# Optimization experiments

Measured on AMD Instinct MI355X. Metric: run time of the kernel, lower is better.

Reference implementation:

```python
import jax, jax.numpy as jnp
import numpy as np
import math

B, S, D, H, DFF, V = 8, 512, 512, 8, 2048, 32000
EPS = 1e-5

def _pe_table(max_len, d):
    pos = jnp.arange(max_len, dtype=jnp.float32)[:, None]
    i = jnp.arange(d)
    exponent = (2 * (i // 2)).astype(jnp.float32) / d
    angle = pos / jnp.power(10000.0, exponent)[None, :]
    return jnp.where(i % 2 == 0, jnp.sin(angle), jnp.cos(angle))

def _ln(x, g, b):
    mu = jnp.mean(x, -1, keepdims=True)
    var = jnp.mean((x - mu) ** 2, -1, keepdims=True)
    return g * (x - mu) * jax.lax.rsqrt(var + EPS) + b

def setup_inputs() -> dict:
    key = jax.random.key(0)
    ks = jax.random.split(key, 16)
    n = jax.random.normal
    return {
        "tokens": jax.random.randint(ks[0], (B, S), 0, V, dtype=jnp.int32),
        "emb": n(ks[1], (V, D), jnp.float32),
        "pe": _pe_table(1000, D),
        "Wq": n(ks[2], (H, D, D), jnp.float32), "bq": jnp.zeros((H, D), jnp.float32),
        "Wk": n(ks[3], (H, D, D), jnp.float32), "bk": jnp.zeros((H, D), jnp.float32),
        "Wv": n(ks[4], (H, D, D), jnp.float32), "bv": jnp.zeros((H, D), jnp.float32),
        "Wo": n(ks[5], (H * D, D), jnp.float32), "bo": jnp.zeros((D,), jnp.float32),
        "g1": jnp.ones((D,), jnp.float32), "be1": jnp.zeros((D,), jnp.float32),
        "W1": n(ks[6], (D, DFF), jnp.float32), "b1": jnp.zeros((DFF,), jnp.float32),
        "W2": n(ks[7], (DFF, D), jnp.float32), "b2": jnp.zeros((D,), jnp.float32),
        "g2": jnp.ones((D,), jnp.float32), "be2": jnp.zeros((D,), jnp.float32),
        "Wf": n(ks[8], (D, V), jnp.float32), "bf": jnp.zeros((V,), jnp.float32),
    }

def reference(tokens, emb, pe, Wq, bq, Wk, bk, Wv, bv, Wo, bo, g1, be1,
              W1, b1, W2, b2, g2, be2, Wf, bf):
    x = emb[tokens] + pe[:tokens.shape[1]]  # [B,S,D]
    res = x
    # input-level "causal" mask over (seq, feature) plane, as in the source
    mask = jnp.triu(jnp.ones((S, D), dtype=bool), k=1)
    xm = jnp.where(mask, 0.0, x)
    scale = 1.0 / math.sqrt(D)
    q = jnp.einsum('bsd,hde->hbse', xm, Wq) + bq[:, None, None, :]
    k = jnp.einsum('bsd,hde->hbse', xm, Wk) + bk[:, None, None, :]
    v = jnp.einsum('bsd,hde->hbse', xm, Wv) + bv[:, None, None, :]
    attn = jax.nn.softmax(jnp.einsum('hbse,hbte->hbst', q, k) * scale, axis=-1)
    o = jnp.einsum('hbst,hbte->hbse', attn, v)  # [H,B,S,D]
    cat = o.transpose(1, 2, 0, 3).reshape(B, S, H * D)  # matches torch.cat head order
    x = _ln(res + (cat @ Wo + bo), g1, be1)
    res = x
    ff = jax.nn.relu(x @ W1 + b1) @ W2 + b2
    x = _ln(res + ff, g2, be2)
    return x @ Wf + bf  # [B,S,V]
```

## Files before the change

### kernel.cpp

```cpp
#include <hip/hip_runtime.h>

typedef unsigned short u16;
typedef unsigned int u32;
typedef short s16x8 __attribute__((ext_vector_type(8)));
typedef __bf16 bf16x8 __attribute__((ext_vector_type(8)));
typedef float f32x4 __attribute__((ext_vector_type(4)));

#define DEVI static __device__ __forceinline__

#define SS 512
#define DD 512
#define NFF 2048
#define VV 32000
#define MTOT 4096
#define HD 4096
#define KC 1536

DEVI float bf2f(u16 h){ return __uint_as_float(((u32)h) << 16); }
DEVI u16 f2bf(float f){
  u32 u = __float_as_uint(f);
  return (u16)((u + 0x7FFFu + ((u >> 16) & 1u)) >> 16);
}
DEVI float ldf(const void* p, long i, int isbf){
  return isbf ? bf2f(((const u16*)p)[i]) : ((const float*)p)[i];
}

DEVI f32x4 mfma16(s16x8 a, s16x8 b, f32x4 c){
  return __builtin_amdgcn_mfma_f32_16x16x32_bf16(
      __builtin_bit_cast(bf16x8, a), __builtin_bit_cast(bf16x8, b), c, 0, 0, 0);
}

typedef const __attribute__((address_space(1))) unsigned int* gup;
typedef __attribute__((address_space(3))) unsigned int* lup;
DEVI void gload16(const void* g, void* l){
  __builtin_amdgcn_global_load_lds((gup)g, (lup)l, 16, 0, 0);
}

DEVI float wave_redsum(float v){
  #pragma unroll
  for (int off = 32; off > 0; off >>= 1) v += __shfl_xor(v, off, 64);
  return v;
}

__global__ void k_dflag(const void* pe, int* flag){
  flag[0] = (*(const u32*)pe == 0x3F800000u) ? 1 : 0;
}

__global__ __launch_bounds__(256) void k_embed(
    const int* __restrict__ tok, const void* __restrict__ emb, const void* __restrict__ pe,
    float* __restrict__ x, u16* __restrict__ xm2, const int* __restrict__ dflag)
{
  int isbf = dflag[0];
  int blk = blockIdx.x;
  int s = blk & (SS - 1);
  int t = tok[blk];
  long rb = (long)blk * 1024;
  for (int d = threadIdx.x; d < DD; d += 256){
    float e = ldf(emb, (long)t * DD + d, isbf) + ldf(pe, (long)s * DD + d, isbf);
    x[(long)blk * DD + d] = e;
    float m = (d <= s) ? e : 0.f;
    u16 hi = f2bf(m);
    u16 lo = f2bf(m - bf2f(hi));
    xm2[rb + d] = hi;
    xm2[rb + 512 + d] = lo;
  }
}

__global__ __launch_bounds__(256) void k_wsplitT(
    const void* __restrict__ Wq, const void* __restrict__ Wk,
    u16* __restrict__ Wq2, u16* __restrict__ Wk2, const int* __restrict__ dflag)
{
  int isbf = dflag[0];
  int zz = blockIdx.z;
  const void* in = (zz < 8) ? Wq : Wk;
  u16* out = (zz < 8) ? Wq2 : Wk2;
  int z = zz & 7;
  long zin = (long)z * DD * DD;
  long zout = (long)z * DD * 1024;
  __shared__ float t[32][33];
  int e0 = blockIdx.x * 32, d0 = blockIdx.y * 32;
  int tx = threadIdx.x & 31, ty = threadIdx.x >> 5;
  #pragma unroll
  for (int i = 0; i < 4; i++){
    int d = ty + i * 8;
    t[d][tx] = ldf(in, zin + (long)(d0 + d) * DD + e0 + tx, isbf);
  }
  __syncthreads();
  #pragma unroll
  for (int i = 0; i < 4; i++){
    int e = ty + i * 8;
    float v = t[tx][e];
    u16 hi = f2bf(v);
    u16 lo = f2bf(v - bf2f(hi));
    long ob = zout + (long)(e0 + e) * 1024 + d0 + tx;
    out[ob] = hi;
    out[ob + 512] = lo;
  }
}

__global__ __launch_bounds__(256) void k_transAll(
    const void* __restrict__ Wv, const void* __restrict__ Wo,
    const void* __restrict__ W1, const void* __restrict__ W2,
    const void* __restrict__ Wf,
    u16* __restrict__ WvT, u16* __restrict__ WoT, u16* __restrict__ W1T,
    u16* __restrict__ W2T, u16* __restrict__ WfT, const int* __restrict__ dflag)
{
  int isbf = dflag[0];
  int f = blockIdx.x;
  const void* in; u16* out; int R, C, gx, loc;
  if (f < 2048)      { in = Wv; out = WvT; R = 512;  C = 512;   gx = 16;   loc = f; }
  else if (f < 4096) { in = Wo; out = WoT; R = 4096; C = 512;   gx = 16;   loc = f - 2048; }
  else if (f < 5120) { in = W1; out = W1T; R = 512;  C = 2048;  gx = 64;   loc = f - 4096; }
  else if (f < 6144) { in = W2; out = W2T; R = 2048; C = 512;   gx = 16;   loc = f - 5120; }
  else               { in = Wf; out = WfT; R = 512;  C = 32000; gx = 1000; loc = f - 6144; }
  int bx = loc % gx;
  int rest = loc / gx;
  int gy = R >> 5;
  int by = rest % gy, z = rest / gy;
  long zo = (long)z * R * C;
  __shared__ float t[32][33];
  int c0 = bx * 32, r0 = by * 32;
  int tx = threadIdx.x & 31, ty = threadIdx.x >> 5;
  #pragma unroll
  for (int i = 0; i < 4; i++){
    int r = ty + i * 8;
    t[r][tx] = ldf(in, zo + (long)(r0 + r) * C + c0 + tx, isbf);
  }
  __syncthreads();
  #pragma unroll
  for (int i = 0; i < 4; i++){
    int c = ty + i * 8;
    out[zo + (long)(c0 + c) * R + r0 + tx] = f2bf(t[tx][c]);
  }
}

enum { EP_QK = 0, EP_SCALE = 1, EP_VT = 2, EP_CAT = 3, EP_OUT = 4,
       EP_F32RES = 5, EP_RELU = 6 };

template<int MODE, bool GSWAP>
__global__ __launch_bounds__(256) void k_mfma(
    const u16* __restrict__ A, long sA, int lda,
    const u16* __restrict__ Bt, long sB,
    void* __restrict__ Cv,
    const void* __restrict__ bias,
    const float* __restrict__ res,
    int K, int ldc, float scale,
    const int* __restrict__ dflag)
{
  int isbf = dflag[0];
  int z = blockIdx.z;
  const u16* Ab = A + (long)z * sA;
  const u16* Bb = Bt + (long)z * sB;
  __shared__ __align__(16) u16 As[2][4][128][8];
  __shared__ __align__(16) u16 Bs[2][4][128][8];
  int m0 = (GSWAP ? blockIdx.x : blockIdx.y) * 128;
  int n0 = (GSWAP ? blockIdx.y : blockIdx.x) * 128;
  int tid = threadIdx.x;
  int lane = tid & 63, w = tid >> 6;
  int wr = (w >> 1) * 64, wc = (w & 1) * 64;
  int l15 = lane & 15, l4 = lane >> 4;
  int s0 = w * 64 + lane;
  int ar0 = s0 & 127, ak0 = s0 >> 7;
  int ak1 = ak0 + 2;
  f32x4 zero = {0.f, 0.f, 0.f, 0.f};
  f32x4 acc[4][4];
  #pragma unroll
  for (int i = 0; i < 4; i++)
    #pragma unroll
    for (int j = 0; j < 4; j++) acc[i][j] = zero;

  const long arow0 = (long)(m0 + ar0) * lda;
  const long brow0 = (long)(n0 + ar0) * K;

  #define STAGE(buf, k0) do{ \
    u16* AsF = &As[buf][0][0][0]; \
    u16* BsF = &Bs[buf][0][0][0]; \
    gload16(Ab + arow0 + (k0) + ak0 * 8, AsF + (long)(w * 64) * 8); \
    gload16(Ab + arow0 + (k0) + ak1 * 8, AsF + (long)(256 + w * 64) * 8); \
    gload16(Bb + brow0 + (k0) + ak0 * 8, BsF + (long)(w * 64) * 8); \
    gload16(Bb + brow0 + (k0) + ak1 * 8, BsF + (long)(256 + w * 64) * 8); \
  }while(0)

  #define COMPUTE(buf) do{ \
    s16x8 af[4], bfr[4]; \
    _Pragma("unroll") \
    for (int i = 0; i < 4; i++) af[i] = *(const s16x8*)&As[buf][l4][wr + i * 16 + l15][0]; \
    _Pragma("unroll") \
    for (int j = 0; j < 4; j++) bfr[j] = *(const s16x8*)&Bs[buf][l4][wc + j * 16 + l15][0]; \
    _Pragma("unroll") \
    for (int i = 0; i < 4; i++) \
      _Pragma("unroll") \
      for (int j = 0; j < 4; j++) \
        acc[i][j] = mfma16(af[i], bfr[j], acc[i][j]); \
  }while(0)

  STAGE(0, 0);
  __syncthreads();
  for (int k0 = 0; k0 < K; k0 += 64){
    STAGE(1, k0 + 32);
    COMPUTE(0);
    __syncthreads();
    if (k0 + 64 < K) STAGE(0, k0 + 64);
    COMPUTE(1);
    __syncthreads();
  }
  #undef STAGE
  #undef COMPUTE

  int mbase = m0 + wr + l4 * 4;
  int nbase = n0 + wc + l15;
  if constexpr (MODE == EP_F32RES){
    float* C = (float*)Cv;
    #pragma unroll
    for (int j = 0; j < 4; j++){
      int n = nbase + j * 16;
      float badd = ldf(bias, n, isbf);
      #pragma unroll
      for (int i = 0; i < 4; i++)
        #pragma unroll
        for (int r = 0; r < 4; r++){
          long a = (long)(mbase + i * 16 + r) * ldc + n;
          C[a] = acc[i][j][r] + badd + res[a];
        }
    }
  } else if constexpr (MODE == EP_RELU){
    u16* C = (u16*)Cv;
    #pragma unroll
    for (int j = 0; j < 4; j++){
      int n = nbase + j * 16;
      float badd = ldf(bias, n, isbf);
      #pragma unroll
      for (int i = 0; i < 4; i++)
        #pragma unroll
        for (int r = 0; r < 4; r++)
          C[(long)(mbase + i * 16 + r) * ldc + n] = f2bf(fmaxf(acc[i][j][r] + badd, 0.f));
    }
  }
}

template<int MODE, bool GSWAP, int AMAP, int BMAP>
__global__ __launch_bounds__(512, 2) void k_mfma2(
    const u16* __restrict__ A, long sA, int lda,
    const u16* __restrict__ Bt, long sB, int ldb,
    void* __restrict__ Cv,
    const void* __restrict__ bias,
    const float* __restrict__ res,
    int K, int ldc, float scale,
    const int* __restrict__ dflag)
{
  int isbf = dflag[0];
  int z = blockIdx.z;
  const u16* Ab = A + (long)z * sA;
  const u16* Bb = Bt + (long)z * sB;
  __shared__ __align__(16) char smem[65536];
  u16* SA = (u16*)smem;
  u16* SB = (u16*)(smem + 32768);
  int m0 = (GSWAP ? blockIdx.x : blockIdx.y) * 256;
  int n0 = (GSWAP ? blockIdx.y : blockIdx.x) * 256;
  int tid = threadIdx.x;
  int lane = tid & 63, w = tid >> 6;
  int wm = (w >> 2) * 128, wn = (w & 3) * 64;
  int l15 = lane & 15, l4 = lane >> 4;
  int row = tid & 255, ob = tid >> 8;
  f32x4 zero = {0.f, 0.f, 0.f, 0.f};
  f32x4 acc[8][4];
  #pragma unroll
  for (int i = 0; i < 8; i++)
    #pragma unroll
    for (int j = 0; j < 4; j++) acc[i][j] = zero;

  const long arow0 = (long)(m0 + row) * lda;
  const long brow0 = (long)(n0 + row) * ldb;

  #define STAGE2(buf, k0_) do{ \
    int ka = (AMAP == 1) ? ((k0_) < 512 ? (k0_) : (k0_) - 512) \
           : (AMAP == 2) ? ((k0_) < 1024 ? (k0_) : (k0_) - 1024) : (k0_); \
    int kb = (BMAP == 1) ? ((k0_) < 512 ? (k0_) : (k0_) - 512) \
           : (BMAP == 2) ? ((k0_) < 1024 ? (k0_) : (k0_) - 1024) : (k0_); \
    gload16(Ab + arow0 + ka + ob * 8,       SA + ((buf) * 8192 + (ob * 256 + row) * 8)); \
    gload16(Ab + arow0 + ka + (ob + 2) * 8, SA + ((buf) * 8192 + ((ob + 2) * 256 + row) * 8)); \
    gload16(Bb + brow0 + kb + ob * 8,       SB + ((buf) * 8192 + (ob * 256 + row) * 8)); \
    gload16(Bb + brow0 + kb + (ob + 2) * 8, SB + ((buf) * 8192 + ((ob + 2) * 256 + row) * 8)); \
  }while(0)

  #define COMPUTE2(buf) do{ \
    s16x8 bfr[4]; \
    _Pragma("unroll") \
    for (int j = 0; j < 4; j++) \
      bfr[j] = *(const s16x8*)(SB + ((buf) * 8192 + l4 * 2048 + (wn + j * 16 + l15) * 8)); \
    _Pragma("unroll") \
    for (int i = 0; i < 8; i++){ \
      s16x8 af = *(const s16x8*)(SA + ((buf) * 8192 + l4 * 2048 + (wm + i * 16 + l15) * 8)); \
      _Pragma("unroll") \
      for (int j = 0; j < 4; j++) \
        acc[i][j] = mfma16(af, bfr[j], acc[i][j]); \
    } \
  }while(0)

  STAGE2(0, 0);
  __syncthreads();
  for (int k0 = 0; k0 < K; k0 += 64){
    STAGE2(1, k0 + 32);
    COMPUTE2(0);
    __syncthreads();
    if (k0 + 64 < K) STAGE2(0, k0 + 64);
    COMPUTE2(1);
    __syncthreads();
  }
  #undef STAGE2
  #undef COMPUTE2

  int mbase = m0 + wm + l4 * 4;
  int nbase = n0 + wn + l15;
  if constexpr (MODE == EP_CAT){
    u16* C = (u16*)Cv;
    int h = z >> 3, b = z & 7;
    #pragma unroll
    for (int i = 0; i < 8; i++){
      int s = mbase + i * 16;
      #pragma unroll
      for (int j = 0; j < 4; j++){
        int n = nbase + j * 16;
        #pragma unroll
        for (int r = 0; r < 4; r++)
          C[((long)b * SS + s + r) * HD + (long)h * DD + n] = f2bf(acc[i][j][r]);
      }
    }
  }
}

__global__ __launch_bounds__(512, 2) void k_out8(
    const u16* __restrict__ A, const u16* __restrict__ Bt,
    float* __restrict__ O, const void* __restrict__ bias,
    int NT, const int* __restrict__ dflag)
{
  int isbf = dflag[0];
  __shared__ __align__(16) char smem[131072];
  u16* SM = (u16*)smem;
  int f = blockIdx.x + gridDim.x * blockIdx.y;
  int qx = (gridDim.x * gridDim.y) >> 3;
  int L = (f & 7) * qx + (f >> 3);
  int m0 = (L % gridDim.x) * 256;
  int n0 = (L / gridDim.x) * 256;
  int tid = threadIdx.x;
  int lane = tid & 63, w = tid >> 6;
  int wm = (w >> 2) * 128, wn = (w & 3) * 64;
  int l15 = lane & 15, l4 = lane >> 4;
  f32x4 zero = {0.f, 0.f, 0.f, 0.f};
  f32x4 acc[8][4];
  #pragma unroll
  for (int i = 0; i < 8; i++)
    #pragma unroll
    for (int j = 0; j < 4; j++) acc[i][j] = zero;

  int rr = tid & 127, kc1 = tid >> 7;

  #define STAGEU(c, Tt, u) do{ \
    const u16* gb = (((u) & 1) == 0) ? A : Bt; \
    int base0 = (((u) & 1) == 0) ? m0 : n0; \
    int r2 = ((u) >> 1) * 128 + rr; \
    long gsrc = (long)(base0 + r2) * 512 + (Tt) * 64; \
    u16* lb = SM + (c) * 32768 + ((((u) & 1) == 0) ? 0 : 16384); \
    gload16(gb + gsrc + kc1 * 8,       lb + (kc1 * 256 + r2) * 8); \
    gload16(gb + gsrc + (kc1 + 4) * 8, lb + ((kc1 + 4) * 256 + r2) * 8); \
  }while(0)

  STAGEU(0, 0, 0); STAGEU(0, 0, 1); STAGEU(0, 0, 2); STAGEU(0, 0, 3);

  int cur = 0;
  for (int T = 0; T < NT; T++){
    int nxt = cur ^ 1;
    int more = (T + 1 < NT);
    s16x8 af[8];
    #pragma unroll
    for (int q = 0; q < 4; q++){
      if (more) STAGEU(nxt, T + 1, q);
      if (q == 0){
        if (more) asm volatile("s_waitcnt vmcnt(2)" ::: "memory");
        else      asm volatile("s_waitcnt vmcnt(0)" ::: "memory");
      }
      __builtin_amdgcn_s_barrier();
      __builtin_amdgcn_sched_barrier(0);
      int ks = q >> 1, jh = q & 1;
      if (jh == 0){
        #pragma unroll
        for (int i = 0; i < 8; i++)
          af[i] = *(const s16x8*)(SM + cur * 32768 +
                    ((ks * 4 + l4) * 256 + (wm + i * 16 + l15)) * 8);
      }
      s16x8 b0 = *(const s16x8*)(SM + cur * 32768 + 16384 +
                    ((ks * 4 + l4) * 256 + (wn + (jh * 2) * 16 + l15)) * 8);
      s16x8 b1 = *(const s16x8*)(SM + cur * 32768 + 16384 +
                    ((ks * 4 + l4) * 256 + (wn + (jh * 2 + 1) * 16 + l15)) * 8);
      __builtin_amdgcn_s_setprio(1);
      #pragma unroll
      for (int i = 0; i < 8; i++){
        acc[i][jh * 2]     = mfma16(af[i], b0, acc[i][jh * 2]);
        acc[i][jh * 2 + 1] = mfma16(af[i], b1, acc[i][jh * 2 + 1]);
      }
      __builtin_amdgcn_s_setprio(0);
    }
    __builtin_amdgcn_s_barrier();
    __builtin_amdgcn_sched_barrier(0);
    cur = nxt;
  }
  #undef STAGEU

  float* ldsT = (float*)smem;
  const int RST = 260;
  int hs16 = (w >> 2) * 16;
  float badd[4];
  #pragma unroll
  for (int j = 0; j < 4; j++) badd[j] = ldf(bias, n0 + wn + j * 16 + l15, isbf);
  #pragma unroll
  for (int i = 0; i < 8; i++){
    __syncthreads();
    #pragma unroll
    for (int j = 0; j < 4; j++){
      int col = wn + j * 16 + l15;
      #pragma unroll
      for (int r = 0; r < 4; r++)
        ldsT[(hs16 + l4 * 4 + r) * RST + col] = acc[i][j][r] + badd[j];
    }
    __syncthreads();
    #pragma unroll
    for (int p = 0; p < 4; p++){
      int chunk = tid + p * 512;
      int lr = chunk >> 6, c4 = chunk & 63;
      int gm = m0 + (lr >> 4) * 128 + i * 16 + (lr & 15);
      f32x4 v = *(f32x4*)&ldsT[lr * RST + c4 * 4];
      __builtin_nontemporal_store(v, (f32x4*)&O[(long)gm * VV + n0 + c4 * 4]);
    }
  }
}

__global__ __launch_bounds__(512, 2) void k_proj(
    const u16* __restrict__ xm2,
    const u16* __restrict__ Wq2, const u16* __restrict__ Wk2, const u16* __restrict__ WvT,
    u16* __restrict__ q2, u16* __restrict__ k2, u16* __restrict__ vT,
    const void* __restrict__ bq, const void* __restrict__ bk, const void* __restrict__ bv,
    const int* __restrict__ dflag)
{
  int isbf = dflag[0];
  int zz = blockIdx.z;
  int z, ldb, K, amap, bmap, mode;
  const u16* Bb; const void* bias; u16* C;
  if (zz < 16){
    mode = 0; z = zz & 7;
    Bb = (zz < 8 ? Wq2 : Wk2) + (long)z * 524288;
    ldb = 1024; K = KC; amap = 1; bmap = 2;
    bias = (zz < 8) ? bq : bk;
    C = (zz < 8) ? q2 : k2;
  } else {
    mode = 1; z = zz - 16;
    Bb = WvT + (long)z * 262144;
    ldb = 512; K = 512; amap = 0; bmap = 0;
    bias = bv;
    C = vT;
  }
  const u16* Ab = xm2;
  __shared__ __align__(16) char smem[65536];
  u16* SA = (u16*)smem;
  u16* SB = (u16*)(smem + 32768);
  int m0 = blockIdx.y * 256;
  int n0 = blockIdx.x * 256;
  int tid = threadIdx.x;
  int lane = tid & 63, w = tid >> 6;
  int wm = (w >> 2) * 128, wn = (w & 3) * 64;
  int l15 = lane & 15, l4 = lane >> 4;
  int row = tid & 255, ob = tid >> 8;
  f32x4 zero = {0.f, 0.f, 0.f, 0.f};
  f32x4 acc[8][4];
  #pragma unroll
  for (int i = 0; i < 8; i++)
    #pragma unroll
    for (int j = 0; j < 4; j++) acc[i][j] = zero;

  const long arow0 = (long)(m0 + row) * 1024;
  const long brow0 = (long)(n0 + row) * ldb;

  #define STAGEP(buf, k0_) do{ \
    int ka = (amap == 1) ? ((k0_) < 512 ? (k0_) : (k0_) - 512) : (k0_); \
    int kb = (bmap == 2) ? ((k0_) < 1024 ? (k0_) : (k0_) - 1024) : (k0_); \
    gload16(Ab + arow0 + ka + ob * 8,       SA + ((buf) * 8192 + (ob * 256 + row) * 8)); \
    gload16(Ab + arow0 + ka + (ob + 2) * 8, SA + ((buf) * 8192 + ((ob + 2) * 256 + row) * 8)); \
    gload16(Bb + brow0 + kb + ob * 8,       SB + ((buf) * 8192 + (ob * 256 + row) * 8)); \
    gload16(Bb + brow0 + kb + (ob + 2) * 8, SB + ((buf) * 8192 + ((ob + 2) * 256 + row) * 8)); \
  }while(0)

  #define COMPUTEP(buf) do{ \
    s16x8 bfr[4]; \
    _Pragma("unroll") \
    for (int j = 0; j < 4; j++) \
      bfr[j] = *(const s16x8*)(SB + ((buf) * 8192 + l4 * 2048 + (wn + j * 16 + l15) * 8)); \
    _Pragma("unroll") \
    for (int i = 0; i < 8; i++){ \
      s16x8 af = *(const s16x8*)(SA + ((buf) * 8192 + l4 * 2048 + (wm + i * 16 + l15) * 8)); \
      _Pragma("unroll") \
      for (int j = 0; j < 4; j++) \
        acc[i][j] = mfma16(af, bfr[j], acc[i][j]); \
    } \
  }while(0)

  STAGEP(0, 0);
  __syncthreads();
  for (int k0 = 0; k0 < K; k0 += 64){
    STAGEP(1, k0 + 32);
    COMPUTEP(0);
    __syncthreads();
    if (k0 + 64 < K) STAGEP(0, k0 + 64);
    COMPUTEP(1);
    __syncthreads();
  }
  #undef STAGEP
  #undef COMPUTEP

  int mbase = m0 + wm + l4 * 4;
  int nbase = n0 + wn + l15;
  if (mode == 0){
    u16* Cz = C + (long)z * ((long)MTOT * 1024);
    #pragma unroll
    for (int j = 0; j < 4; j++){
      int n = nbase + j * 16;
      float badd = ldf(bias, (long)z * DD + n, isbf);
      #pragma unroll
      for (int i = 0; i < 8; i++)
        #pragma unroll
        for (int r = 0; r < 4; r++){
          float qv = acc[i][j][r] + badd;
          u16 hi = f2bf(qv);
          u16 lo = f2bf(qv - bf2f(hi));
          long rb = (long)(mbase + i * 16 + r) * 1024;
          Cz[rb + n] = hi;
          Cz[rb + 512 + n] = lo;
        }
    }
  } else {
    #pragma unroll
    for (int i = 0; i < 8; i++){
      int mrow = mbase + i * 16;
      int b = mrow >> 9, s = mrow & (SS - 1);
      #pragma unroll
      for (int j = 0; j < 4; j++){
        int n = nbase + j * 16;
        float badd = ldf(bias, (long)z * DD + n, isbf);
        ushort4 pk;
        pk.x = f2bf(acc[i][j][0] + badd); pk.y = f2bf(acc[i][j][1] + badd);
        pk.z = f2bf(acc[i][j][2] + badd); pk.w = f2bf(acc[i][j][3] + badd);
        *(ushort4*)&C[((long)(z * 8 + b) * DD + n) * SS + s] = pk;
      }
    }
  }
}

template<int AMAP, int BMAP>
__global__ __launch_bounds__(512, 2) void k_fsm(
    const u16* __restrict__ A, long sA, int lda,
    const u16* __restrict__ Bt, long sB, int ldb,
    u16* __restrict__ P, int K, float scale,
    const int* __restrict__ dflag)
{
  int z = blockIdx.z;
  const u16* Ab = A + (long)z * sA;
  const u16* Bb = Bt + (long)z * sB;
  __shared__ __align__(16) char smem[81920];
  u16* SA = (u16*)smem;
  u16* SB = (u16*)(smem + 16384);
  int m0 = blockIdx.x * 128;
  int tid = threadIdx.x;
  int lane = tid & 63, w = tid >> 6;
  int wn = w * 64;
  int l15 = lane & 15, l4 = lane >> 4;
  f32x4 zero = {0.f, 0.f, 0.f, 0.f};
  f32x4 acc[8][4];
  #pragma unroll
  for (int i = 0; i < 8; i++)
    #pragma unroll
    for (int j = 0; j < 4; j++) acc[i][j] = zero;

  const long arow0 = (long)(m0 + (tid & 127)) * lda;
  const int akc = tid >> 7;
  const long brow0 = (long)tid * ldb;

  #define STAGEF(buf, k0_) do{ \
    int ka = (AMAP == 1) ? ((k0_) < 512 ? (k0_) : (k0_) - 512) \
           : (AMAP == 2) ? ((k0_) < 1024 ? (k0_) : (k0_) - 1024) : (k0_); \
    int kb = (BMAP == 1) ? ((k0_) < 512 ? (k0_) : (k0_) - 512) \
           : (BMAP == 2) ? ((k0_) < 1024 ? (k0_) : (k0_) - 1024) : (k0_); \
    gload16(Ab + arow0 + ka + akc * 8, SA + ((buf) * 4096 + tid * 8)); \
    gload16(Bb + brow0 + kb + 0,  SB + ((buf) * 16384 + (0 * 512 + tid) * 8)); \
    gload16(Bb + brow0 + kb + 8,  SB + ((buf) * 16384 + (1 * 512 + tid) * 8)); \
    gload16(Bb + brow0 + kb + 16, SB + ((buf) * 16384 + (2 * 512 + tid) * 8)); \
    gload16(Bb + brow0 + kb + 24, SB + ((buf) * 16384 + (3 * 512 + tid) * 8)); \
  }while(0)

  #define COMPUTEF(buf) do{ \
    s16x8 bfr[4]; \
    _Pragma("unroll") \
    for (int j = 0; j < 4; j++) \
      bfr[j] = *(const s16x8*)(SB + ((buf) * 16384 + l4 * 4096 + (wn + j * 16 + l15) * 8)); \
    _Pragma("unroll") \
    for (int i = 0; i < 8; i++){ \
      s16x8 af = *(const s16x8*)(SA + ((buf) * 4096 + l4 * 1024 + (i * 16 + l15) * 8)); \
      _Pragma("unroll") \
      for (int j = 0; j < 4; j++) \
        acc[i][j] = mfma16(af, bfr[j], acc[i][j]); \
    } \
  }while(0)

  STAGEF(0, 0);
  __syncthreads();
  for (int k0 = 0; k0 < K; k0 += 64){
    STAGEF(1, k0 + 32);
    COMPUTEF(0);
    __syncthreads();
    if (k0 + 64 < K) STAGEF(0, k0 + 64);
    COMPUTEF(1);
    __syncthreads();
  }
  #undef STAGEF
  #undef COMPUTEF

  float* sred = (float*)smem;
  float* srow = (float*)(smem + 4096);

  #pragma unroll
  for (int i = 0; i < 8; i++)
    #pragma unroll
    for (int j = 0; j < 4; j++)
      acc[i][j] *= scale;

  #pragma unroll
  for (int i = 0; i < 8; i++)
    #pragma unroll
    for (int r = 0; r < 4; r++){
      float m = fmaxf(fmaxf(acc[i][0][r], acc[i][1][r]),
                      fmaxf(acc[i][2][r], acc[i][3][r]));
      #pragma unroll
      for (int off = 1; off < 16; off <<= 1) m = fmaxf(m, __shfl_xor(m, off, 64));
      if (l15 == 0) sred[w * 128 + l4 * 4 + i * 16 + r] = m;
    }
  __syncthreads();
  if (tid < 128){
    float m = sred[tid];
    #pragma unroll
    for (int w2 = 1; w2 < 8; w2++) m = fmaxf(m, sred[w2 * 128 + tid]);
    srow[tid] = m;
  }
  __syncthreads();
  #pragma unroll
  for (int i = 0; i < 8; i++)
    #pragma unroll
    for (int r = 0; r < 4; r++){
      float rm = srow[l4 * 4 + i * 16 + r];
      float s = 0.f;
      #pragma unroll
      for (int j = 0; j < 4; j++){
        float e = expf(acc[i][j][r] - rm);
        acc[i][j][r] = e;
        s += e;
      }
      #pragma unroll
      for (int off = 1; off < 16; off <<= 1) s += __shfl_xor(s, off, 64);
      if (l15 == 0) sred[w * 128 + l4 * 4 + i * 16 + r] = s;
    }
  __syncthreads();
  if (tid < 128){
    float s = 0.f;
    #pragma unroll
    for (int w2 = 0; w2 < 8; w2++) s += sred[w2 * 128 + tid];
    srow[tid] = 1.f / s;
  }
  __syncthreads();
  u16* Pz = P + (long)z * ((long)SS * SS);
  u16* pb = (u16*)(smem + 8192);
  const int PST = 520;
  #pragma unroll
  for (int ii = 0; ii < 4; ii++){
    __syncthreads();
    #pragma unroll
    for (int s2 = 0; s2 < 2; s2++){
      int i = ii * 2 + s2;
      #pragma unroll
      for (int r = 0; r < 4; r++){
        int rl = l4 * 4 + i * 16 + r;
        float inv = srow[rl];
        #pragma unroll
        for (int j = 0; j < 4; j++)
          pb[(s2 * 16 + l4 * 4 + r) * PST + wn + j * 16 + l15] = f2bf(acc[i][j][r] * inv);
      }
    }
    __syncthreads();
    #pragma unroll
    for (int p = 0; p < 8; p++){
      int chunk = tid + p * 512;
      int lr = chunk >> 7, c8 = chunk & 127;
      ushort4 v = *(ushort4*)&pb[lr * PST + c8 * 4];
      *(ushort4*)&Pz[(long)(m0 + ii * 32 + lr) * SS + c8 * 4] = v;
    }
  }
}

template<bool WF32>
__global__ __launch_bounds__(256) void k_ln(
    const float* __restrict__ X, const void* __restrict__ g, const void* __restrict__ be,
    u16* __restrict__ Yb, float* __restrict__ Yf, const int* __restrict__ dflag)
{
  int isbf = dflag[0];
  int row = blockIdx.x * 4 + (threadIdx.x >> 6);
  int lane = threadIdx.x & 63;
  const float* p = X + (long)row * DD + lane * 8;
  float4 v0 = *(const float4*)p;
  float4 v1 = *(const float4*)(p + 4);
  float v[8] = {v0.x, v0.y, v0.z, v0.w, v1.x, v1.y, v1.z, v1.w};
  float s = 0.f;
  #pragma unroll
  for (int i = 0; i < 8; i++) s += v[i];
  s = wave_redsum(s);
  float mu = s * (1.f / DD);
  float d_[8], sq = 0.f;
  #pragma unroll
  for (int i = 0; i < 8; i++){ d_[i] = v[i] - mu; sq += d_[i] * d_[i]; }
  sq = wave_redsum(sq);
  float rs = 1.f / sqrtf(sq * (1.f / DD) + 1e-5f);
  #pragma unroll
  for (int i = 0; i < 8; i++){
    int dd = lane * 8 + i;
    float y = ldf(g, dd, isbf) * d_[i] * rs + ldf(be, dd, isbf);
    Yb[(long)row * DD + dd] = f2bf(y);
    if (WF32) Yf[(long)row * DD + dd] = y;
  }
}

extern "C" void kernel_launch(void* const* d_in, const int* in_sizes, int n_in,
                              void* d_out, int out_size, void* d_ws, size_t ws_size,
                              hipStream_t stream)
{
  const int* tokens = (const int*)d_in[0];
  const void* emb = d_in[1];
  const void* pe  = d_in[2];
  const void* Wq  = d_in[3];
  const void* bq  = d_in[4];
  const void* Wk  = d_in[5];
  const void* bk  = d_in[6];
  const void* Wv  = d_in[7];
  const void* bv  = d_in[8];
  const void* Wo  = d_in[9];
  const void* bo  = d_in[10];
  const void* g1  = d_in[11];
  const void* be1 = d_in[12];
  const void* W1  = d_in[13];
  const void* b1  = d_in[14];
  const void* W2  = d_in[15];
  const void* b2  = d_in[16];
  const void* g2  = d_in[17];
  const void* be2 = d_in[18];
  const void* Wf  = d_in[19];
  const void* bfb = d_in[20];
  float* out = (float*)d_out;
  char* ws = (char*)d_ws;
  char* DO = (char*)d_out;

  const size_t MB = 1ull << 20;
  int* dflag = (int*)ws;
  u16* x2b   = (u16*)(ws + 1 * MB);
  u16* WfT   = (u16*)(ws + 8 * MB);

  float* x    = (float*)(DO + 0 * MB);
  u16*   xm2  = (u16*)(DO + 8 * MB);
  u16*   Wq2  = (u16*)(DO + 16 * MB);
  u16*   Wk2  = (u16*)(DO + 24 * MB);
  u16*   WvT  = (u16*)(DO + 32 * MB);
  u16*   WoT  = (u16*)(DO + 36 * MB);
  u16*   W1T  = (u16*)(DO + 40 * MB);
  u16*   W2T  = (u16*)(DO + 42 * MB);
  u16*   q2   = (u16*)(DO + 48 * MB);
  u16*   k2   = (u16*)(DO + 112 * MB);
  u16*   attn = (u16*)(DO + 240 * MB);
  u16*   vT   = (u16*)(DO + 272 * MB);
  u16*   cat  = (u16*)(DO + 304 * MB);
  float* proj = (float*)(DO + 336 * MB);
  float* x1f  = (float*)(DO + 344 * MB);
  u16*   x1b  = (u16*)(DO + 352 * MB);
  u16*   ff1  = (u16*)(DO + 356 * MB);
  float* ff2  = (float*)(DO + 372 * MB);

  const float scale = 0.04419417382415922f;
  const long HSL = 262144;
  const long QSL = 524288;

  k_dflag<<<1, 1, 0, stream>>>(pe, dflag);
  k_embed<<<dim3(4096), 256, 0, stream>>>(tokens, emb, pe, x, xm2, dflag);

  k_wsplitT<<<dim3(16, 16, 16), 256, 0, stream>>>(Wq, Wk, Wq2, Wk2, dflag);
  k_transAll<<<dim3(22144), 256, 0, stream>>>(
      Wv, Wo, W1, W2, Wf, WvT, WoT, W1T, W2T, WfT, dflag);

  k_proj<<<dim3(2, 16, 24), 512, 0, stream>>>(
      xm2, Wq2, Wk2, WvT, q2, k2, vT, bq, bk, bv, dflag);

  k_fsm<1, 2><<<dim3(4, 1, 64), 512, 0, stream>>>(
      q2, QSL, 1024, k2, QSL, 1024, attn, KC, scale, dflag);

  k_mfma2<EP_CAT, false, 0, 0><<<dim3(2, 2, 64), 512, 0, stream>>>(
      attn, HSL, SS, vT, HSL, 512, cat, nullptr, nullptr, SS, 0, 0.f, dflag);

  k_mfma<EP_F32RES, false><<<dim3(4, 32, 1), 256, 0, stream>>>(
      cat, 0, HD, WoT, 0, proj, bo, x, HD, DD, 0.f, dflag);
  k_ln<true><<<dim3(1024), 256, 0, stream>>>(proj, g1, be1, x1b, x1f, dflag);

  k_mfma<EP_RELU, false><<<dim3(16, 32, 1), 256, 0, stream>>>(
      x1b, 0, DD, W1T, 0, ff1, b1, nullptr, DD, NFF, 0.f, dflag);
  k_mfma<EP_F32RES, false><<<dim3(4, 32, 1), 256, 0, stream>>>(
      ff1, 0, NFF, W2T, 0, ff2, b2, x1f, NFF, DD, 0.f, dflag);
  k_ln<false><<<dim3(1024), 256, 0, stream>>>(ff2, g2, be2, x2b, nullptr, dflag);

  k_out8<<<dim3(16, 125, 1), 512, 0, stream>>>(x2b, WfT, out, bfb, 8, dflag);
}
```

Baseline: 970.4 us.

## Restructure QKV projection GEMM into 64-wide K tiles with interleaved async staging

The projection kernel now stages 64-element K tiles into a 128KB double-buffered LDS region, with the next tile's loads split into four quarter-stages interleaved with the MFMA sub-steps of the current tile. Explicit vmcnt waits, raw s_barrier, sched_barrier and setprio replace the previous two-stage 32-wide loop with full __syncthreads. The aim is to hide global-load latency behind compute and to halve the number of loop iterations and barriers. The larger LDS footprint (128KB per block) may drop occupancy to one block per CU despite launch_bounds(512,2), and the hand-tuned vmcnt counts depend on how the compiler emits the loads.

```diff
diff --git a/kernel.cpp b/kernel.cpp
--- a/kernel.cpp
+++ b/kernel.cpp
@@ -434,7 +434,7 @@
   }
 }
 
-__global__ __launch_bounds__(512, 2) void k_proj(
+__global__ __launch_bounds__(512, 2) void k_proj8(
     const u16* __restrict__ xm2,
     const u16* __restrict__ Wq2, const u16* __restrict__ Wk2, const u16* __restrict__ WvT,
     u16* __restrict__ q2, u16* __restrict__ k2, u16* __restrict__ vT,
@@ -443,32 +443,30 @@
 {
   int isbf = dflag[0];
   int zz = blockIdx.z;
-  int z, ldb, K, amap, bmap, mode;
+  int z, ldb, NT, mode;
   const u16* Bb; const void* bias; u16* C;
   if (zz < 16){
     mode = 0; z = zz & 7;
     Bb = (zz < 8 ? Wq2 : Wk2) + (long)z * 524288;
-    ldb = 1024; K = KC; amap = 1; bmap = 2;
+    ldb = 1024; NT = 24;
     bias = (zz < 8) ? bq : bk;
     C = (zz < 8) ? q2 : k2;
   } else {
     mode = 1; z = zz - 16;
     Bb = WvT + (long)z * 262144;
-    ldb = 512; K = 512; amap = 0; bmap = 0;
+    ldb = 512; NT = 8;
     bias = bv;
     C = vT;
   }
   const u16* Ab = xm2;
-  __shared__ __align__(16) char smem[65536];
-  u16* SA = (u16*)smem;
-  u16* SB = (u16*)(smem + 32768);
+  __shared__ __align__(16) char smem[131072];
+  u16* SM = (u16*)smem;
   int m0 = blockIdx.y * 256;
   int n0 = blockIdx.x * 256;
   int tid = threadIdx.x;
   int lane = tid & 63, w = tid >> 6;
   int wm = (w >> 2) * 128, wn = (w & 3) * 64;
   int l15 = lane & 15, l4 = lane >> 4;
-  int row = tid & 255, ob = tid >> 8;
   f32x4 zero = {0.f, 0.f, 0.f, 0.f};
   f32x4 acc[8][4];
   #pragma unroll
@@ -476,44 +474,65 @@
     #pragma unroll
     for (int j = 0; j < 4; j++) acc[i][j] = zero;
 
-  const long arow0 = (long)(m0 + row) * 1024;
-  const long brow0 = (long)(n0 + row) * ldb;
-
-  #define STAGEP(buf, k0_) do{ \
-    int ka = (amap == 1) ? ((k0_) < 512 ? (k0_) : (k0_) - 512) : (k0_); \
-    int kb = (bmap == 2) ? ((k0_) < 1024 ? (k0_) : (k0_) - 1024) : (k0_); \
-    gload16(Ab + arow0 + ka + ob * 8,       SA + ((buf) * 8192 + (ob * 256 + row) * 8)); \
-    gload16(Ab + arow0 + ka + (ob + 2) * 8, SA + ((buf) * 8192 + ((ob + 2) * 256 + row) * 8)); \
-    gload16(Bb + brow0 + kb + ob * 8,       SB + ((buf) * 8192 + (ob * 256 + row) * 8)); \
-    gload16(Bb + brow0 + kb + (ob + 2) * 8, SB + ((buf) * 8192 + ((ob + 2) * 256 + row) * 8)); \
+  int rr = tid & 127, kc1 = tid >> 7;
+
+  #define KA8(Tt) (mode == 0 ? (((Tt) * 64 < 512) ? (Tt) * 64 : (Tt) * 64 - 512) : (Tt) * 64)
+  #define KB8(Tt) (mode == 0 ? (((Tt) * 64 < 1024) ? (Tt) * 64 : (Tt) * 64 - 1024) : (Tt) * 64)
+
+  #define STAGEU(c, Tt, u) do{ \
+    const u16* gb = (((u) & 1) == 0) ? Ab : Bb; \
+    long rs = (((u) & 1) == 0) ? 1024 : (long)ldb; \
+    int base0 = (((u) & 1) == 0) ? m0 : n0; \
+    int tk = (((u) & 1) == 0) ? KA8(Tt) : KB8(Tt); \
+    int r2 = ((u) >> 1) * 128 + rr; \
+    long gsrc = (long)(base0 + r2) * rs + tk; \
+    u16* lb = SM + (c) * 32768 + ((((u) & 1) == 0) ? 0 : 16384); \
+    gload16(gb + gsrc + kc1 * 8,       lb + (kc1 * 256 + r2) * 8); \
+    gload16(gb + gsrc + (kc1 + 4) * 8, lb + ((kc1 + 4) * 256 + r2) * 8); \
   }while(0)
 
-  #define COMPUTEP(buf) do{ \
-    s16x8 bfr[4]; \
-    _Pragma("unroll") \
-    for (int j = 0; j < 4; j++) \
-      bfr[j] = *(const s16x8*)(SB + ((buf) * 8192 + l4 * 2048 + (wn + j * 16 + l15) * 8)); \
-    _Pragma("unroll") \
-    for (int i = 0; i < 8; i++){ \
-      s16x8 af = *(const s16x8*)(SA + ((buf) * 8192 + l4 * 2048 + (wm + i * 16 + l15) * 8)); \
-      _Pragma("unroll") \
-      for (int j = 0; j < 4; j++) \
-        acc[i][j] = mfma16(af, bfr[j], acc[i][j]); \
-    } \
-  }while(0)
-
-  STAGEP(0, 0);
-  __syncthreads();
-  for (int k0 = 0; k0 < K; k0 += 64){
-    STAGEP(1, k0 + 32);
-    COMPUTEP(0);
-    __syncthreads();
-    if (k0 + 64 < K) STAGEP(0, k0 + 64);
-    COMPUTEP(1);
-    __syncthreads();
-  }
-  #undef STAGEP
-  #undef COMPUTEP
+  STAGEU(0, 0, 0); STAGEU(0, 0, 1); STAGEU(0, 0, 2); STAGEU(0, 0, 3);
+
+  int cur = 0;
+  for (int T = 0; T < NT; T++){
+    int nxt = cur ^ 1;
+    int more = (T + 1 < NT);
+    s16x8 af[8];
+    #pragma unroll
+    for (int q = 0; q < 4; q++){
+      if (more) STAGEU(nxt, T + 1, q);
+      if (q == 0){
+        if (more) asm volatile("s_waitcnt vmcnt(2)" ::: "memory");
+        else      asm volatile("s_waitcnt vmcnt(0)" ::: "memory");
+      }
+      __builtin_amdgcn_s_barrier();
+      __builtin_amdgcn_sched_barrier(0);
+      int ks = q >> 1, jh = q & 1;
+      if (jh == 0){
+        #pragma unroll
+        for (int i = 0; i < 8; i++)
+          af[i] = *(const s16x8*)(SM + cur * 32768 +
+                    ((ks * 4 + l4) * 256 + (wm + i * 16 + l15)) * 8);
+      }
+      s16x8 b0 = *(const s16x8*)(SM + cur * 32768 + 16384 +
+                    ((ks * 4 + l4) * 256 + (wn + (jh * 2) * 16 + l15)) * 8);
+      s16x8 b1 = *(const s16x8*)(SM + cur * 32768 + 16384 +
+                    ((ks * 4 + l4) * 256 + (wn + (jh * 2 + 1) * 16 + l15)) * 8);
+      __builtin_amdgcn_s_setprio(1);
+      #pragma unroll
+      for (int i = 0; i < 8; i++){
+        acc[i][jh * 2]     = mfma16(af[i], b0, acc[i][jh * 2]);
+        acc[i][jh * 2 + 1] = mfma16(af[i], b1, acc[i][jh * 2 + 1]);
+      }
+      __builtin_amdgcn_s_setprio(0);
+    }
+    __builtin_amdgcn_s_barrier();
+    __builtin_amdgcn_sched_barrier(0);
+    cur = nxt;
+  }
+  #undef STAGEU
+  #undef KA8
+  #undef KB8
 
   int mbase = m0 + wm + l4 * 4;
   int nbase = n0 + wn + l15;
@@ -796,7 +815,7 @@
   k_transAll<<<dim3(22144), 256, 0, stream>>>(
       Wv, Wo, W1, W2, Wf, WvT, WoT, W1T, W2T, WfT, dflag);
 
-  k_proj<<<dim3(2, 16, 24), 512, 0, stream>>>(
+  k_proj8<<<dim3(2, 16, 24), 512, 0, stream>>>(
       xm2, Wq2, Wk2, WvT, q2, k2, vT, bq, bk, bv, dflag);
 
   k_fsm<1, 2><<<dim3(4, 1, 64), 512, 0, stream>>>(
```

After: 929.5 us. 4.2% less time.
